# Optimization experiments

Hardware: AMD Instinct MI355X
Metric: run time of the kernel (lower is better)

Reference implementation:

```python
import jax, jax.numpy as jnp
import numpy as np

N = 100_000          # nodes
E = 1_600_000        # edges (avg degree 16)
NODE_SCA, NODE_VEC = 4, 3
EDGE_SCA, EDGE_VEC = 6, 3
OUT_SCA, OUT_VEC = 16, 16
CUTOFF = 10.0
EPS = 1e-6
SLOPE_VN = 0.2       # VNLeakyReLU negative slope (SurfGen default)
SLOPE_SCA = 0.01     # nn.LeakyReLU default


def setup_inputs() -> dict:
    key = jax.random.key(0)
    ks = jax.random.split(key, 22)
    rn = lambda k, s: jax.random.normal(k, s, dtype=jnp.float32)
    return {
        # forward args
        'node_sca': rn(ks[0], (N, NODE_SCA)),
        'node_vec': rn(ks[1], (N, NODE_VEC, 3)),
        'edge_sca': rn(ks[2], (E, EDGE_SCA)),
        'edge_vec': rn(ks[3], (E, EDGE_VEC, 3)),
        'gds_dist': jax.random.uniform(ks[4], (E,), dtype=jnp.float32) * 12.0,
        'edge_index': jax.random.randint(ks[5], (2, E), 0, N),
        # message projections (Linear weights stored [in,out])
        'W_nss': rn(ks[6], (NODE_SCA, OUT_SCA)) * 0.3, 'b_nss': rn(ks[7], (OUT_SCA,)) * 0.1,
        'W_ess': rn(ks[8], (EDGE_SCA, OUT_SCA)) * 0.3, 'b_ess': rn(ks[9], (OUT_SCA,)) * 0.1,
        'W_nsv': rn(ks[10], (NODE_SCA, OUT_SCA)) * 0.3, 'b_nsv': rn(ks[11], (OUT_SCA,)) * 0.1,
        'W_esv': rn(ks[12], (EDGE_SCA, OUT_SCA)) * 0.3, 'b_esv': rn(ks[13], (OUT_SCA,)) * 0.1,
        'W_nvv': rn(ks[14], (NODE_VEC, OUT_VEC)) * 0.3,   # VNLinear (no bias)
        'W_evv': rn(ks[15], (EDGE_VEC, OUT_VEC)) * 0.3,
        # GVPerceptronVN(16,16,16,16): GVLinear (dim_hid = 16) + VN LeakyReLU
        'W_lv':  rn(ks[16], (OUT_VEC, OUT_VEC)) * 0.25,   # lin_vector   (no bias)
        'W_lv2': rn(ks[17], (OUT_VEC, OUT_VEC)) * 0.25,   # lin_vector2  (no bias)
        'W_ls':  rn(ks[18], (OUT_VEC + OUT_SCA, OUT_SCA)) * 0.25,  # lin_scalar (no bias)
        'W_gate': rn(ks[19], (OUT_SCA, OUT_VEC)) * 0.25, 'b_gate': rn(ks[20], (OUT_VEC,)) * 0.1,
        'W_dir': rn(ks[21], (OUT_VEC, OUT_VEC)) * 0.25,   # VNLeakyReLU direction (no bias)
    }


def vn_linear(x, W):
    # x: [n, c_in, 3], W: [c_in, c_out] -> [n, c_out, 3]
    return jnp.einsum('nci,co->noi', x, W)


def reference(node_sca, node_vec, edge_sca, edge_vec, gds_dist, edge_index,
              W_nss, b_nss, W_ess, b_ess, W_nsv, b_nsv, W_esv, b_esv,
              W_nvv, W_evv, W_lv, W_lv2, W_ls, W_gate, b_gate, W_dir):
    src = edge_index[0]
    num_nodes = node_sca.shape[0]

    # cosine cutoff coefficient
    coeff = 0.5 * (jnp.cos(gds_dist * (jnp.pi / CUTOFF)) + 1.0)
    coeff = coeff * (gds_dist <= CUTOFF) * (gds_dist >= 0.0)  # [E]

    # scalar message: gather node proj, mix with edge proj, cutoff-weight
    node_ss = node_sca @ W_nss + b_nss                          # [N,16]
    edge_ss = edge_sca @ W_ess + b_ess                          # [E,16]
    msg_sca = node_ss[src] * edge_ss * coeff[:, None]           # [E,16]

    # vector message
    node_vv = vn_linear(node_vec, W_nvv)                        # [N,16,3]
    edge_vv = vn_linear(edge_vec, W_evv)                        # [E,16,3]
    node_sv = node_sca @ W_nsv + b_nsv                          # [N,16]
    edge_sv = edge_sca @ W_esv + b_esv                          # [E,16]
    msg_vec = (node_vv[src] * edge_sv[:, :, None]
               + node_sv[src][:, :, None] * edge_vv) * coeff[:, None, None]  # [E,16,3]

    # scatter_sum into source nodes (matches original's edge_index[0])
    aggr_sca = jax.ops.segment_sum(msg_sca, src, num_segments=num_nodes)  # [N,16]
    aggr_vec = jax.ops.segment_sum(msg_vec, src, num_segments=num_nodes)  # [N,16,3]

    # --- GVPerceptronVN: GVLinear ---
    v_inter = vn_linear(aggr_vec, W_lv)                          # [N,16,3]
    v_norm = jnp.sqrt(jnp.sum(v_inter * v_inter, axis=-1))       # [N,16]
    out_sca = jnp.concatenate([v_norm, aggr_sca], axis=-1) @ W_ls  # [N,16]
    out_vec = vn_linear(v_inter, W_lv2)                          # [N,16,3]
    gate = jax.nn.sigmoid(out_sca @ W_gate + b_gate)[:, :, None]
    out_vec = gate * out_vec

    # --- VNLeakyReLU on vectors ---
    d = vn_linear(out_vec, W_dir)                                # [N,16,3]
    dot = jnp.sum(out_vec * d, axis=-1, keepdims=True)
    mask = (dot >= 0).astype(out_vec.dtype)
    d_norm_sq = jnp.sum(d * d, axis=-1, keepdims=True)
    out_vec = SLOPE_VN * out_vec + (1.0 - SLOPE_VN) * (
        mask * out_vec + (1.0 - mask) * (out_vec - (dot / (d_norm_sq + EPS)) * d))

    # LeakyReLU on scalars
    out_sca = jnp.where(out_sca >= 0, out_sca, SLOPE_SCA * out_sca)
    return out_sca, out_vec
```

## Files before the change

### kernel.cpp

```cpp
#include <hip/hip_runtime.h>
#include <hip/hip_fp16.h>
#include <math.h>

#define CUTOFF_F 10.0f
#define PI_OVER_CUTOFF 0.31415926535897931f
#define KCAP 64
#define KCAP3 32

__global__ __launch_bounds__(256) void bucket_scatter(
    const float* __restrict__ edge_sca,
    const float* __restrict__ edge_vec,
    const float* __restrict__ gds,
    const int* __restrict__ eidx,
    int* __restrict__ count,
    __half* __restrict__ bucket,
    float* __restrict__ aggr,
    int E)
{
    int e = blockIdx.x * blockDim.x + threadIdx.x;
    if (e >= E) return;

    int src = eidx[e];
    float d = gds[e];
    float c = 0.0f;
    if (d >= 0.0f && d <= CUTOFF_F)
        c = 0.5f * (__cosf(d * PI_OVER_CUTOFF) + 1.0f);

    const float* es = edge_sca + (size_t)e * 6;
    const float* ev = edge_vec + (size_t)e * 9;

    float f[16];
#pragma unroll
    for (int i = 0; i < 6; ++i) f[i] = c * es[i];
    f[6] = c;
#pragma unroll
    for (int i = 0; i < 9; ++i) f[7 + i] = c * ev[i];

    int slot = atomicAdd(&count[src], 1);
    if (slot < KCAP3) {
        union { __half h[16]; uint4 u[2]; } pk;
#pragma unroll
        for (int i = 0; i < 16; ++i) pk.h[i] = __float2half(f[i]);
        uint4* pb = (uint4*)(bucket + ((size_t)src * KCAP3 + slot) * 16);
        pb[0] = pk.u[0];
        pb[1] = pk.u[1];
    } else {
        float* base = aggr + (size_t)src * 16;
#pragma unroll
        for (int i = 0; i < 16; ++i) atomicAdd(base + i, f[i]);
    }
}

__global__ __launch_bounds__(256) void count_edges(
    const int* __restrict__ eidx, int* __restrict__ count,
    int* __restrict__ slotOf, int E)
{
    int e = blockIdx.x * blockDim.x + threadIdx.x;
    if (e >= E) return;
    int src = eidx[e];
    slotOf[e] = atomicAdd(&count[src], 1);
}

__global__ __launch_bounds__(256) void scan_block_sums(
    const int* __restrict__ count, int* __restrict__ blockSums, int N)
{
    __shared__ int sdata[256];
    int t = threadIdx.x;
    int i = blockIdx.x * 256 + t;
    sdata[t] = (i < N) ? count[i] : 0;
    __syncthreads();
    for (int off = 128; off > 0; off >>= 1) {
        if (t < off) sdata[t] += sdata[t + off];
        __syncthreads();
    }
    if (t == 0) blockSums[blockIdx.x] = sdata[0];
}

__global__ __launch_bounds__(1024) void scan_exclusive_small(
    int* __restrict__ blockSums, int M)
{
    __shared__ int s[1024];
    int t = threadIdx.x;
    int orig = (t < M) ? blockSums[t] : 0;
    s[t] = orig;
    __syncthreads();
    for (int off = 1; off < 1024; off <<= 1) {
        int v = (t >= off) ? s[t - off] : 0;
        __syncthreads();
        s[t] += v;
        __syncthreads();
    }
    if (t < M) blockSums[t] = s[t] - orig;
}

__global__ __launch_bounds__(256) void scan_final(
    const int* __restrict__ count, const int* __restrict__ blockSums,
    int* __restrict__ offsets, int N)
{
    __shared__ int s[256];
    int t = threadIdx.x;
    int i = blockIdx.x * 256 + t;
    int orig = (i < N) ? count[i] : 0;
    s[t] = orig;
    __syncthreads();
    for (int off = 1; off < 256; off <<= 1) {
        int v = (t >= off) ? s[t - off] : 0;
        __syncthreads();
        s[t] += v;
        __syncthreads();
    }
    if (i < N) offsets[i] = s[t] - orig + blockSums[blockIdx.x];
}

__global__ __launch_bounds__(256) void scatter_payload(
    const float* __restrict__ edge_sca, const float* __restrict__ edge_vec,
    const float* __restrict__ gds, const int* __restrict__ eidx,
    const int* __restrict__ slotOf, const int* __restrict__ offsets,
    __half* __restrict__ payload, int E)
{
    int e = blockIdx.x * blockDim.x + threadIdx.x;
    if (e >= E) return;
    int src = eidx[e];
    float d = gds[e];
    float c = 0.0f;
    if (d >= 0.0f && d <= CUTOFF_F)
        c = 0.5f * (__cosf(d * PI_OVER_CUTOFF) + 1.0f);
    const float* es = edge_sca + (size_t)e * 6;
    const float* ev = edge_vec + (size_t)e * 9;
    union { __half h[16]; uint4 u[2]; } pk;
#pragma unroll
    for (int i = 0; i < 6; ++i) pk.h[i] = __float2half(c * es[i]);
    pk.h[6] = __float2half(c);
#pragma unroll
    for (int i = 0; i < 9; ++i) pk.h[7 + i] = __float2half(c * ev[i]);
    uint4* pb = (uint4*)(payload + (size_t)(offsets[src] + slotOf[e]) * 16);
    pb[0] = pk.u[0];
    pb[1] = pk.u[1];
}

__global__ __launch_bounds__(256) void fill_buckets(
    const int* __restrict__ eidx, int* __restrict__ count,
    int* __restrict__ bucket, int E)
{
    int e = blockIdx.x * blockDim.x + threadIdx.x;
    if (e >= E) return;
    int src = eidx[e];
    int slot = atomicAdd(&count[src], 1);
    if (slot < KCAP) bucket[src * KCAP + slot] = e;
}

__global__ __launch_bounds__(256) void edge_aggregate(
    const float* __restrict__ edge_sca, const float* __restrict__ edge_vec,
    const float* __restrict__ gds, const int* __restrict__ eidx,
    float* __restrict__ aggr, int E)
{
    int e = blockIdx.x * blockDim.x + threadIdx.x;
    if (e >= E) return;
    int src = eidx[e];
    float d = gds[e];
    float coeff = 0.0f;
    if (d >= 0.0f && d <= CUTOFF_F)
        coeff = 0.5f * (__cosf(d * PI_OVER_CUTOFF) + 1.0f);
    float* base = aggr + (size_t)src * 16;
    const float* es = edge_sca + (size_t)e * 6;
    const float* ev = edge_vec + (size_t)e * 9;
#pragma unroll
    for (int c = 0; c < 6; ++c) atomicAdd(base + c, coeff * es[c]);
    atomicAdd(base + 6, coeff);
#pragma unroll
    for (int k = 0; k < 9; ++k) atomicAdd(base + 7 + k, coeff * ev[k]);
}

__global__ __launch_bounds__(256) void node_fused(
    const float* __restrict__ node_sca,
    const float* __restrict__ node_vec,
    const float* __restrict__ edge_sca,
    const float* __restrict__ edge_vec,
    const float* __restrict__ gds,
    const int* __restrict__ count,
    const int* __restrict__ bucket,
    const int* __restrict__ offsets,
    const __half* __restrict__ payload,
    const float* __restrict__ aggr,
    const float* __restrict__ W_nss, const float* __restrict__ b_nss,
    const float* __restrict__ W_ess, const float* __restrict__ b_ess,
    const float* __restrict__ W_nsv, const float* __restrict__ b_nsv,
    const float* __restrict__ W_esv, const float* __restrict__ b_esv,
    const float* __restrict__ W_nvv, const float* __restrict__ W_evv,
    const float* __restrict__ W_lv,  const float* __restrict__ W_lv2,
    const float* __restrict__ W_ls,
    const float* __restrict__ W_gate, const float* __restrict__ b_gate,
    const float* __restrict__ W_dir,
    float* __restrict__ out,
    int N, int mode)
{
    __shared__ float sW_nss[64],  sb_nss[16];
    __shared__ float sW_ess[96],  sb_ess[16];
    __shared__ float sW_nsv[64],  sb_nsv[16];
    __shared__ float sW_esv[96],  sb_esv[16];
    __shared__ float sW_nvv[48],  sW_evv[48];
    __shared__ float sW_lv[256],  sW_lv2[256];
    __shared__ float sW_ls[512];
    __shared__ float sW_gate[256], sb_gate[16];
    __shared__ float sW_dir[256];

    __shared__ float s_in  [16 * 33];
    __shared__ float s_avec[16 * 49];
    __shared__ float s_cat [16 * 33];
    __shared__ float s_vint[16 * 49];
    __shared__ float s_osca[16 * 17];
    __shared__ float s_ovec[16 * 49];

    const int t = threadIdx.x;
    {
        for (int i = t; i < 64;  i += 256) { sW_nss[i] = W_nss[i]; sW_nsv[i] = W_nsv[i]; }
        for (int i = t; i < 96;  i += 256) { sW_ess[i] = W_ess[i]; sW_esv[i] = W_esv[i]; }
        for (int i = t; i < 48;  i += 256) { sW_nvv[i] = W_nvv[i]; sW_evv[i] = W_evv[i]; }
        for (int i = t; i < 256; i += 256) {
            sW_lv[i]   = W_lv[i];
            sW_lv2[i]  = W_lv2[i];
            sW_gate[i] = W_gate[i];
            sW_dir[i]  = W_dir[i];
        }
        for (int i = t; i < 512; i += 256) sW_ls[i] = W_ls[i];
        if (t < 16) {
            sb_nss[t]  = b_nss[t];
            sb_ess[t]  = b_ess[t];
            sb_nsv[t]  = b_nsv[t];
            sb_esv[t]  = b_esv[t];
            sb_gate[t] = b_gate[t];
        }
    }

    const int slot = t >> 4;
    const int o    = t & 15;
    const int n    = blockIdx.x * 16 + slot;
    const bool valid = (n < N);

    if (valid) {
        if (o < 4) s_in[slot * 33 + o]     = node_sca[(size_t)n * 4 + o];
        if (o < 9) s_in[slot * 33 + 4 + o] = node_vec[(size_t)n * 9 + o];
    }

    if (mode == 3) {
        float a0 = 0.f, a1 = 0.f, a2 = 0.f, a3 = 0.f;
        if (valid) {
            int cnt = count[n];
            if (cnt > KCAP3) cnt = KCAP3;
            const __half* p = payload + (size_t)n * KCAP3 * 16 + o;
            int s = 0;
            for (; s + 3 < cnt; s += 4) {
                a0 += __half2float(p[(s + 0) * 16]);
                a1 += __half2float(p[(s + 1) * 16]);
                a2 += __half2float(p[(s + 2) * 16]);
                a3 += __half2float(p[(s + 3) * 16]);
            }
            for (; s < cnt; ++s)
                a0 += __half2float(p[s * 16]);
            a1 += aggr[(size_t)n * 16 + o];
            s_in[slot * 33 + 13 + o] = (a0 + a1) + (a2 + a3);
        }
    } else if (mode == 2) {
        float a0 = 0.f, a1 = 0.f, a2 = 0.f, a3 = 0.f;
        if (valid) {
            int cnt = count[n];
            const __half* p = payload + (size_t)offsets[n] * 16 + o;
            int s = 0;
            for (; s + 3 < cnt; s += 4) {
                a0 += __half2float(p[(size_t)(s + 0) * 16]);
                a1 += __half2float(p[(size_t)(s + 1) * 16]);
                a2 += __half2float(p[(size_t)(s + 2) * 16]);
                a3 += __half2float(p[(size_t)(s + 3) * 16]);
            }
            for (; s < cnt; ++s)
                a0 += __half2float(p[(size_t)s * 16]);
            s_in[slot * 33 + 13 + o] = (a0 + a1) + (a2 + a3);
        }
    } else if (mode == 1) {
        float acc = 0.0f;
        int cnt = valid ? count[n] : 0;
        if (cnt > KCAP) cnt = KCAP;
        const int* bk = bucket + (size_t)n * KCAP;
        for (int s = 0; s < cnt; ++s) {
            int e = bk[s];
            float d = gds[e];
            float coeff = 0.0f;
            if (d >= 0.0f && d <= CUTOFF_F)
                coeff = 0.5f * (__cosf(d * PI_OVER_CUTOFF) + 1.0f);
            float feat;
            if (o < 6)       feat = edge_sca[(size_t)e * 6 + o];
            else if (o == 6) feat = 1.0f;
            else             feat = edge_vec[(size_t)e * 9 + (o - 7)];
            acc += coeff * feat;
        }
        if (valid) s_in[slot * 33 + 13 + o] = acc;
    } else {
        if (valid) s_in[slot * 33 + 13 + o] = aggr[(size_t)n * 16 + o];
    }
    __syncthreads();

    const float* in = s_in + slot * 33;

    float nss = sb_nss[o], nsv = sb_nsv[o];
#pragma unroll
    for (int c = 0; c < 4; ++c) {
        float x = in[c];
        nss += x * sW_nss[c * 16 + o];
        nsv += x * sW_nsv[c * 16 + o];
    }
    float nvv0 = 0.f, nvv1 = 0.f, nvv2 = 0.f;
#pragma unroll
    for (int c = 0; c < 3; ++c) {
        float w = sW_nvv[c * 16 + o];
        nvv0 += in[4 + c * 3 + 0] * w;
        nvv1 += in[4 + c * 3 + 1] * w;
        nvv2 += in[4 + c * 3 + 2] * w;
    }
    float cc = in[19];
    float es = cc * sb_ess[o], ev = cc * sb_esv[o];
#pragma unroll
    for (int c = 0; c < 6; ++c) {
        float a = in[13 + c];
        es += a * sW_ess[c * 16 + o];
        ev += a * sW_esv[c * 16 + o];
    }
    float EV0 = 0.f, EV1 = 0.f, EV2 = 0.f;
#pragma unroll
    for (int c = 0; c < 3; ++c) {
        float w = sW_evv[c * 16 + o];
        EV0 += in[20 + c * 3 + 0] * w;
        EV1 += in[20 + c * 3 + 1] * w;
        EV2 += in[20 + c * 3 + 2] * w;
    }

    float asca = nss * es;
    float av0 = nvv0 * ev + nsv * EV0;
    float av1 = nvv1 * ev + nsv * EV1;
    float av2 = nvv2 * ev + nsv * EV2;
    s_avec[slot * 49 + o * 3 + 0] = av0;
    s_avec[slot * 49 + o * 3 + 1] = av1;
    s_avec[slot * 49 + o * 3 + 2] = av2;
    s_cat[slot * 33 + 16 + o] = asca;
    __syncthreads();

    float vi0 = 0.f, vi1 = 0.f, vi2 = 0.f;
#pragma unroll
    for (int c = 0; c < 16; ++c) {
        float w = sW_lv[c * 16 + o];
        const float* a = &s_avec[slot * 49 + c * 3];
        vi0 += a[0] * w; vi1 += a[1] * w; vi2 += a[2] * w;
    }
    float vnorm = sqrtf(vi0 * vi0 + vi1 * vi1 + vi2 * vi2);
    s_vint[slot * 49 + o * 3 + 0] = vi0;
    s_vint[slot * 49 + o * 3 + 1] = vi1;
    s_vint[slot * 49 + o * 3 + 2] = vi2;
    s_cat[slot * 33 + o] = vnorm;
    __syncthreads();

    float osca = 0.f;
#pragma unroll
    for (int c = 0; c < 32; ++c)
        osca += s_cat[slot * 33 + c] * sW_ls[c * 16 + o];
    float ov0 = 0.f, ov1 = 0.f, ov2 = 0.f;
#pragma unroll
    for (int c = 0; c < 16; ++c) {
        float w = sW_lv2[c * 16 + o];
        const float* a = &s_vint[slot * 49 + c * 3];
        ov0 += a[0] * w; ov1 += a[1] * w; ov2 += a[2] * w;
    }
    s_osca[slot * 17 + o] = osca;
    __syncthreads();

    float g = sb_gate[o];
#pragma unroll
    for (int c = 0; c < 16; ++c)
        g += s_osca[slot * 17 + c] * sW_gate[c * 16 + o];
    g = 1.0f / (1.0f + __expf(-g));
    ov0 *= g; ov1 *= g; ov2 *= g;
    s_ovec[slot * 49 + o * 3 + 0] = ov0;
    s_ovec[slot * 49 + o * 3 + 1] = ov1;
    s_ovec[slot * 49 + o * 3 + 2] = ov2;
    __syncthreads();

    float dv0 = 0.f, dv1 = 0.f, dv2 = 0.f;
#pragma unroll
    for (int c = 0; c < 16; ++c) {
        float w = sW_dir[c * 16 + o];
        const float* a = &s_ovec[slot * 49 + c * 3];
        dv0 += a[0] * w; dv1 += a[1] * w; dv2 += a[2] * w;
    }
    float dot = ov0 * dv0 + ov1 * dv1 + ov2 * dv2;
    if (dot < 0.0f) {
        float dn = dv0 * dv0 + dv1 * dv1 + dv2 * dv2;
        float f = 0.8f * dot / (dn + 1e-6f);
        ov0 -= f * dv0; ov1 -= f * dv1; ov2 -= f * dv2;
    }

    if (valid) {
        float so = (osca >= 0.0f) ? osca : 0.01f * osca;
        out[(size_t)n * 16 + o] = so;
        size_t vb = (size_t)N * 16 + (size_t)n * 48 + (size_t)o * 3;
        out[vb + 0] = ov0;
        out[vb + 1] = ov1;
        out[vb + 2] = ov2;
    }
}

extern "C" void kernel_launch(void* const* d_in, const int* in_sizes, int n_in,
                              void* d_out, int out_size, void* d_ws, size_t ws_size,
                              hipStream_t stream)
{
    const float* node_sca = (const float*)d_in[0];
    const float* node_vec = (const float*)d_in[1];
    const float* edge_sca = (const float*)d_in[2];
    const float* edge_vec = (const float*)d_in[3];
    const float* gds      = (const float*)d_in[4];
    const int*   eidx     = (const int*)d_in[5];

    const int N = in_sizes[0] / 4;
    const int E = in_sizes[4];

    int*    count3  = (int*)d_ws;
    float*  aggr3   = (float*)(count3 + N);
    __half* bucket3 = (__half*)(aggr3 + (size_t)N * 16);
    size_t  need3   = (size_t)N * 4 + (size_t)N * 64
                    + (size_t)N * KCAP3 * 16 * sizeof(__half);

    int*    count     = (int*)d_ws;
    int*    offsets   = count + N;
    int*    blockSums = offsets + N;
    int*    slotOf    = blockSums + 1024;
    size_t  hdr_bytes = ((size_t)(2 * N + 1024 + E) * 4 + 63) & ~(size_t)63;
    __half* payload   = (__half*)((char*)d_ws + hdr_bytes);
    size_t  need_csr  = hdr_bytes + (size_t)E * 16 * sizeof(__half);
    size_t  need_bkt  = (size_t)N * (1 + KCAP) * sizeof(int);

    const int nBlocksN = (N + 255) / 256;

    int mode;
    if (ws_size >= need3)                          mode = 3;
    else if (ws_size >= need_csr && nBlocksN <= 1024) mode = 2;
    else if (ws_size >= need_bkt)                  mode = 1;
    else                                           mode = 0;

    int* bucket = count + N;
    float* aggr = (float*)d_ws;

    if (mode == 3) {
        hipMemsetAsync(count3, 0, (size_t)N * 4 + (size_t)N * 64, stream);
        bucket_scatter<<<(E + 255) / 256, 256, 0, stream>>>(
            edge_sca, edge_vec, gds, eidx, count3, bucket3, aggr3, E);
        node_fused<<<(N + 15) / 16, 256, 0, stream>>>(
            node_sca, node_vec, edge_sca, edge_vec, gds,
            count3, bucket, offsets, bucket3, aggr3,
            (const float*)d_in[6],  (const float*)d_in[7],
            (const float*)d_in[8],  (const float*)d_in[9],
            (const float*)d_in[10], (const float*)d_in[11],
            (const float*)d_in[12], (const float*)d_in[13],
            (const float*)d_in[14], (const float*)d_in[15],
            (const float*)d_in[16], (const float*)d_in[17],
            (const float*)d_in[18],
            (const float*)d_in[19], (const float*)d_in[20],
            (const float*)d_in[21],
            (float*)d_out, N, 3);
        return;
    }

    if (mode == 2) {
        hipMemsetAsync(count, 0, (size_t)N * sizeof(int), stream);
        count_edges<<<(E + 255) / 256, 256, 0, stream>>>(eidx, count, slotOf, E);
        scan_block_sums<<<nBlocksN, 256, 0, stream>>>(count, blockSums, N);
        scan_exclusive_small<<<1, 1024, 0, stream>>>(blockSums, nBlocksN);
        scan_final<<<nBlocksN, 256, 0, stream>>>(count, blockSums, offsets, N);
        scatter_payload<<<(E + 255) / 256, 256, 0, stream>>>(
            edge_sca, edge_vec, gds, eidx, slotOf, offsets, payload, E);
    } else if (mode == 1) {
        hipMemsetAsync(count, 0, (size_t)N * sizeof(int), stream);
        fill_buckets<<<(E + 255) / 256, 256, 0, stream>>>(eidx, count, bucket, E);
    } else {
        hipMemsetAsync(aggr, 0, (size_t)N * 16 * sizeof(float), stream);
        edge_aggregate<<<(E + 255) / 256, 256, 0, stream>>>(
            edge_sca, edge_vec, gds, eidx, aggr, E);
    }

    node_fused<<<(N + 15) / 16, 256, 0, stream>>>(
        node_sca, node_vec, edge_sca, edge_vec, gds,
        count, bucket, offsets, payload, aggr,
        (const float*)d_in[6],  (const float*)d_in[7],
        (const float*)d_in[8],  (const float*)d_in[9],
        (const float*)d_in[10], (const float*)d_in[11],
        (const float*)d_in[12], (const float*)d_in[13],
        (const float*)d_in[14], (const float*)d_in[15],
        (const float*)d_in[16], (const float*)d_in[17],
        (const float*)d_in[18],
        (const float*)d_in[19], (const float*)d_in[20],
        (const float*)d_in[21],
        (float*)d_out, N, mode);
}
```

Before: 306.0 us.

## Bucket edge ids instead of fp16 payloads and gather features in node kernel

The scatter kernel now writes only the edge id into a per-node bucket of 32 slots, and it skips edges beyond the cutoff before the atomic. It no longer writes a 32-byte fp16 payload per edge. The node kernel stages the ids and cosine coefficients in shared memory and gathers edge_sca and edge_vec rows directly in fp32. This cuts the scatter-side write traffic and the fp16 rounding, at the cost of scattered, uncoalesced gathers of edge features in the node kernel. The CSR and id-only fallback paths are removed.

```diff
diff --git a/kernel.cpp b/kernel.cpp
--- a/kernel.cpp
+++ b/kernel.cpp
@@ -1,152 +1,41 @@
 #include <hip/hip_runtime.h>
-#include <hip/hip_fp16.h>
 #include <math.h>
 
 #define CUTOFF_F 10.0f
 #define PI_OVER_CUTOFF 0.31415926535897931f
-#define KCAP 64
-#define KCAP3 32
-
-__global__ __launch_bounds__(256) void bucket_scatter(
+#define KID 32
+
+__global__ __launch_bounds__(256) void fill_ids(
+    const float* __restrict__ gds,
+    const int* __restrict__ eidx,
     const float* __restrict__ edge_sca,
     const float* __restrict__ edge_vec,
-    const float* __restrict__ gds,
-    const int* __restrict__ eidx,
     int* __restrict__ count,
-    __half* __restrict__ bucket,
+    int* __restrict__ bucket,
     float* __restrict__ aggr,
     int E)
 {
     int e = blockIdx.x * blockDim.x + threadIdx.x;
     if (e >= E) return;
 
-    int src = eidx[e];
     float d = gds[e];
-    float c = 0.0f;
-    if (d >= 0.0f && d <= CUTOFF_F)
-        c = 0.5f * (__cosf(d * PI_OVER_CUTOFF) + 1.0f);
-
-    const float* es = edge_sca + (size_t)e * 6;
-    const float* ev = edge_vec + (size_t)e * 9;
-
-    float f[16];
-#pragma unroll
-    for (int i = 0; i < 6; ++i) f[i] = c * es[i];
-    f[6] = c;
-#pragma unroll
-    for (int i = 0; i < 9; ++i) f[7 + i] = c * ev[i];
-
-    int slot = atomicAdd(&count[src], 1);
-    if (slot < KCAP3) {
-        union { __half h[16]; uint4 u[2]; } pk;
-#pragma unroll
-        for (int i = 0; i < 16; ++i) pk.h[i] = __float2half(f[i]);
-        uint4* pb = (uint4*)(bucket + ((size_t)src * KCAP3 + slot) * 16);
-        pb[0] = pk.u[0];
-        pb[1] = pk.u[1];
-    } else {
-        float* base = aggr + (size_t)src * 16;
-#pragma unroll
-        for (int i = 0; i < 16; ++i) atomicAdd(base + i, f[i]);
-    }
-}
-
-__global__ __launch_bounds__(256) void count_edges(
-    const int* __restrict__ eidx, int* __restrict__ count,
-    int* __restrict__ slotOf, int E)
-{
-    int e = blockIdx.x * blockDim.x + threadIdx.x;
-    if (e >= E) return;
-    int src = eidx[e];
-    slotOf[e] = atomicAdd(&count[src], 1);
-}
-
-__global__ __launch_bounds__(256) void scan_block_sums(
-    const int* __restrict__ count, int* __restrict__ blockSums, int N)
-{
-    __shared__ int sdata[256];
-    int t = threadIdx.x;
-    int i = blockIdx.x * 256 + t;
-    sdata[t] = (i < N) ? count[i] : 0;
-    __syncthreads();
-    for (int off = 128; off > 0; off >>= 1) {
-        if (t < off) sdata[t] += sdata[t + off];
-        __syncthreads();
-    }
-    if (t == 0) blockSums[blockIdx.x] = sdata[0];
-}
-
-__global__ __launch_bounds__(1024) void scan_exclusive_small(
-    int* __restrict__ blockSums, int M)
-{
-    __shared__ int s[1024];
-    int t = threadIdx.x;
-    int orig = (t < M) ? blockSums[t] : 0;
-    s[t] = orig;
-    __syncthreads();
-    for (int off = 1; off < 1024; off <<= 1) {
-        int v = (t >= off) ? s[t - off] : 0;
-        __syncthreads();
-        s[t] += v;
-        __syncthreads();
-    }
-    if (t < M) blockSums[t] = s[t] - orig;
-}
-
-__global__ __launch_bounds__(256) void scan_final(
-    const int* __restrict__ count, const int* __restrict__ blockSums,
-    int* __restrict__ offsets, int N)
-{
-    __shared__ int s[256];
-    int t = threadIdx.x;
-    int i = blockIdx.x * 256 + t;
-    int orig = (i < N) ? count[i] : 0;
-    s[t] = orig;
-    __syncthreads();
-    for (int off = 1; off < 256; off <<= 1) {
-        int v = (t >= off) ? s[t - off] : 0;
-        __syncthreads();
-        s[t] += v;
-        __syncthreads();
-    }
-    if (i < N) offsets[i] = s[t] - orig + blockSums[blockIdx.x];
-}
-
-__global__ __launch_bounds__(256) void scatter_payload(
-    const float* __restrict__ edge_sca, const float* __restrict__ edge_vec,
-    const float* __restrict__ gds, const int* __restrict__ eidx,
-    const int* __restrict__ slotOf, const int* __restrict__ offsets,
-    __half* __restrict__ payload, int E)
-{
-    int e = blockIdx.x * blockDim.x + threadIdx.x;
-    if (e >= E) return;
-    int src = eidx[e];
-    float d = gds[e];
-    float c = 0.0f;
-    if (d >= 0.0f && d <= CUTOFF_F)
-        c = 0.5f * (__cosf(d * PI_OVER_CUTOFF) + 1.0f);
-    const float* es = edge_sca + (size_t)e * 6;
-    const float* ev = edge_vec + (size_t)e * 9;
-    union { __half h[16]; uint4 u[2]; } pk;
-#pragma unroll
-    for (int i = 0; i < 6; ++i) pk.h[i] = __float2half(c * es[i]);
-    pk.h[6] = __float2half(c);
-#pragma unroll
-    for (int i = 0; i < 9; ++i) pk.h[7 + i] = __float2half(c * ev[i]);
-    uint4* pb = (uint4*)(payload + (size_t)(offsets[src] + slotOf[e]) * 16);
-    pb[0] = pk.u[0];
-    pb[1] = pk.u[1];
-}
-
-__global__ __launch_bounds__(256) void fill_buckets(
-    const int* __restrict__ eidx, int* __restrict__ count,
-    int* __restrict__ bucket, int E)
-{
-    int e = blockIdx.x * blockDim.x + threadIdx.x;
-    if (e >= E) return;
+    if (d > CUTOFF_F || d < 0.0f) return;
+
     int src = eidx[e];
     int slot = atomicAdd(&count[src], 1);
-    if (slot < KCAP) bucket[src * KCAP + slot] = e;
+    if (slot < KID) {
+        bucket[(size_t)src * KID + slot] = e;
+    } else {
+        float c = 0.5f * (__cosf(d * PI_OVER_CUTOFF) + 1.0f);
+        const float* es = edge_sca + (size_t)e * 6;
+        const float* ev = edge_vec + (size_t)e * 9;
+        float* base = aggr + (size_t)src * 16;
+#pragma unroll
+        for (int i = 0; i < 6; ++i) atomicAdd(base + i, c * es[i]);
+        atomicAdd(base + 6, c);
+#pragma unroll
+        for (int i = 0; i < 9; ++i) atomicAdd(base + 7 + i, c * ev[i]);
+    }
 }
 
 __global__ __launch_bounds__(256) void edge_aggregate(
@@ -179,8 +68,6 @@
     const float* __restrict__ gds,
     const int* __restrict__ count,
     const int* __restrict__ bucket,
-    const int* __restrict__ offsets,
-    const __half* __restrict__ payload,
     const float* __restrict__ aggr,
     const float* __restrict__ W_nss, const float* __restrict__ b_nss,
     const float* __restrict__ W_ess, const float* __restrict__ b_ess,
@@ -211,6 +98,9 @@
     __shared__ float s_osca[16 * 17];
     __shared__ float s_ovec[16 * 49];
 
+    __shared__ int   s_eid[KID * 17];
+    __shared__ float s_ec [KID * 17];
+
     const int t = threadIdx.x;
     {
         for (int i = t; i < 64;  i += 256) { sW_nss[i] = W_nss[i]; sW_nsv[i] = W_nsv[i]; }
@@ -242,58 +132,33 @@
         if (o < 9) s_in[slot * 33 + 4 + o] = node_vec[(size_t)n * 9 + o];
     }
 
-    if (mode == 3) {
-        float a0 = 0.f, a1 = 0.f, a2 = 0.f, a3 = 0.f;
+    if (mode == 4) {
+        int cnt = 0;
         if (valid) {
-            int cnt = count[n];
-            if (cnt > KCAP3) cnt = KCAP3;
-            const __half* p = payload + (size_t)n * KCAP3 * 16 + o;
-            int s = 0;
-            for (; s + 3 < cnt; s += 4) {
-                a0 += __half2float(p[(s + 0) * 16]);
-                a1 += __half2float(p[(s + 1) * 16]);
-                a2 += __half2float(p[(s + 2) * 16]);
-                a3 += __half2float(p[(s + 3) * 16]);
+            cnt = count[n];
+            if (cnt > KID) cnt = KID;
+            const int* bk = bucket + (size_t)n * KID;
+            for (int s = o; s < cnt; s += 16) {
+                int e = bk[s];
+                float d = gds[e];
+                s_eid[s * 17 + slot] = e;
+                s_ec [s * 17 + slot] = 0.5f * (__cosf(d * PI_OVER_CUTOFF) + 1.0f);
             }
-            for (; s < cnt; ++s)
-                a0 += __half2float(p[s * 16]);
-            a1 += aggr[(size_t)n * 16 + o];
-            s_in[slot * 33 + 13 + o] = (a0 + a1) + (a2 + a3);
         }
-    } else if (mode == 2) {
-        float a0 = 0.f, a1 = 0.f, a2 = 0.f, a3 = 0.f;
+        __syncthreads();
         if (valid) {
-            int cnt = count[n];
-            const __half* p = payload + (size_t)offsets[n] * 16 + o;
-            int s = 0;
-            for (; s + 3 < cnt; s += 4) {
-                a0 += __half2float(p[(size_t)(s + 0) * 16]);
-                a1 += __half2float(p[(size_t)(s + 1) * 16]);
-                a2 += __half2float(p[(size_t)(s + 2) * 16]);
-                a3 += __half2float(p[(size_t)(s + 3) * 16]);
+            float acc = aggr[(size_t)n * 16 + o];
+            const float* fsrc = (o < 6) ? edge_sca : edge_vec;
+            const int    st   = (o < 6) ? 6 : 9;
+            const int    off  = (o < 6) ? o : (o - 7);
+            for (int s = 0; s < cnt; ++s) {
+                int   e = s_eid[s * 17 + slot];
+                float c = s_ec [s * 17 + slot];
+                float f = (o == 6) ? 1.0f : fsrc[(size_t)e * st + off];
+                acc += c * f;
             }
-            for (; s < cnt; ++s)
-                a0 += __half2float(p[(size_t)s * 16]);
-            s_in[slot * 33 + 13 + o] = (a0 + a1) + (a2 + a3);
+            s_in[slot * 33 + 13 + o] = acc;
         }
-    } else if (mode == 1) {
-        float acc = 0.0f;
-        int cnt = valid ? count[n] : 0;
-        if (cnt > KCAP) cnt = KCAP;
-        const int* bk = bucket + (size_t)n * KCAP;
-        for (int s = 0; s < cnt; ++s) {
-            int e = bk[s];
-            float d = gds[e];
-            float coeff = 0.0f;
-            if (d >= 0.0f && d <= CUTOFF_F)
-                coeff = 0.5f * (__cosf(d * PI_OVER_CUTOFF) + 1.0f);
-            float feat;
-            if (o < 6)       feat = edge_sca[(size_t)e * 6 + o];
-            else if (o == 6) feat = 1.0f;
-            else             feat = edge_vec[(size_t)e * 9 + (o - 7)];
-            acc += coeff * feat;
-        }
-        if (valid) s_in[slot * 33 + 13 + o] = acc;
     } else {
         if (valid) s_in[slot * 33 + 13 + o] = aggr[(size_t)n * 16 + o];
     }
@@ -420,39 +285,21 @@
     const int N = in_sizes[0] / 4;
     const int E = in_sizes[4];
 
-    int*    count3  = (int*)d_ws;
-    float*  aggr3   = (float*)(count3 + N);
-    __half* bucket3 = (__half*)(aggr3 + (size_t)N * 16);
-    size_t  need3   = (size_t)N * 4 + (size_t)N * 64
-                    + (size_t)N * KCAP3 * 16 * sizeof(__half);
-
-    int*    count     = (int*)d_ws;
-    int*    offsets   = count + N;
-    int*    blockSums = offsets + N;
-    int*    slotOf    = blockSums + 1024;
-    size_t  hdr_bytes = ((size_t)(2 * N + 1024 + E) * 4 + 63) & ~(size_t)63;
-    __half* payload   = (__half*)((char*)d_ws + hdr_bytes);
-    size_t  need_csr  = hdr_bytes + (size_t)E * 16 * sizeof(__half);
-    size_t  need_bkt  = (size_t)N * (1 + KCAP) * sizeof(int);
-
-    const int nBlocksN = (N + 255) / 256;
-
-    int mode;
-    if (ws_size >= need3)                          mode = 3;
-    else if (ws_size >= need_csr && nBlocksN <= 1024) mode = 2;
-    else if (ws_size >= need_bkt)                  mode = 1;
-    else                                           mode = 0;
-
-    int* bucket = count + N;
-    float* aggr = (float*)d_ws;
-
-    if (mode == 3) {
-        hipMemsetAsync(count3, 0, (size_t)N * 4 + (size_t)N * 64, stream);
-        bucket_scatter<<<(E + 255) / 256, 256, 0, stream>>>(
-            edge_sca, edge_vec, gds, eidx, count3, bucket3, aggr3, E);
+    int*   count4  = (int*)d_ws;
+    float* aggr4   = (float*)(count4 + N);
+    int*   bucket4 = (int*)(aggr4 + (size_t)N * 16);
+    size_t need4   = (size_t)N * 4 + (size_t)N * 64 + (size_t)N * KID * 4;
+
+    float* aggr0  = (float*)d_ws;
+    size_t need0  = (size_t)N * 64;
+
+    if (ws_size >= need4) {
+        hipMemsetAsync(count4, 0, (size_t)N * 4 + (size_t)N * 64, stream);
+        fill_ids<<<(E + 255) / 256, 256, 0, stream>>>(
+            gds, eidx, edge_sca, edge_vec, count4, bucket4, aggr4, E);
         node_fused<<<(N + 15) / 16, 256, 0, stream>>>(
             node_sca, node_vec, edge_sca, edge_vec, gds,
-            count3, bucket, offsets, bucket3, aggr3,
+            count4, bucket4, aggr4,
             (const float*)d_in[6],  (const float*)d_in[7],
             (const float*)d_in[8],  (const float*)d_in[9],
             (const float*)d_in[10], (const float*)d_in[11],
@@ -462,30 +309,17 @@
             (const float*)d_in[18],
             (const float*)d_in[19], (const float*)d_in[20],
             (const float*)d_in[21],
-            (float*)d_out, N, 3);
+            (float*)d_out, N, 4);
         return;
     }
 
-    if (mode == 2) {
-        hipMemsetAsync(count, 0, (size_t)N * sizeof(int), stream);
-        count_edges<<<(E + 255) / 256, 256, 0, stream>>>(eidx, count, slotOf, E);
-        scan_block_sums<<<nBlocksN, 256, 0, stream>>>(count, blockSums, N);
-        scan_exclusive_small<<<1, 1024, 0, stream>>>(blockSums, nBlocksN);
-        scan_final<<<nBlocksN, 256, 0, stream>>>(count, blockSums, offsets, N);
-        scatter_payload<<<(E + 255) / 256, 256, 0, stream>>>(
-            edge_sca, edge_vec, gds, eidx, slotOf, offsets, payload, E);
-    } else if (mode == 1) {
-        hipMemsetAsync(count, 0, (size_t)N * sizeof(int), stream);
-        fill_buckets<<<(E + 255) / 256, 256, 0, stream>>>(eidx, count, bucket, E);
-    } else {
-        hipMemsetAsync(aggr, 0, (size_t)N * 16 * sizeof(float), stream);
-        edge_aggregate<<<(E + 255) / 256, 256, 0, stream>>>(
-            edge_sca, edge_vec, gds, eidx, aggr, E);
-    }
-
+    (void)need0;
+    hipMemsetAsync(aggr0, 0, (size_t)N * 64, stream);
+    edge_aggregate<<<(E + 255) / 256, 256, 0, stream>>>(
+        edge_sca, edge_vec, gds, eidx, aggr0, E);
     node_fused<<<(N + 15) / 16, 256, 0, stream>>>(
         node_sca, node_vec, edge_sca, edge_vec, gds,
-        count, bucket, offsets, payload, aggr,
+        (const int*)d_ws, (const int*)d_ws, aggr0,
         (const float*)d_in[6],  (const float*)d_in[7],
         (const float*)d_in[8],  (const float*)d_in[9],
         (const float*)d_in[10], (const float*)d_in[11],
@@ -495,5 +329,5 @@
         (const float*)d_in[18],
         (const float*)d_in[19], (const float*)d_in[20],
         (const float*)d_in[21],
-        (float*)d_out, N, mode);
+        (float*)d_out, N, 0);
 }
```

Measured after the change: 335.4 us. +9.6%, slower.
